# Kernel tuning notes

Hardware: AMD Instinct MI355X
Metric: run time of the kernel (lower is better)

The kernel has to match this reference:

```python
import jax, jax.numpy as jnp
import numpy as np

BETA = 0.95
THRESHOLD = 1.0
ATAN_ALPHA = 2.0  # snntorch default ATan surrogate slope


@jax.custom_vjp
def spike_fn(u):
    # Heaviside spike with ATan surrogate gradient (snntorch default).
    return (u > 0).astype(u.dtype)

def _spike_fwd(u):
    return spike_fn(u), u

def _spike_bwd(u, g):
    grad = (ATAN_ALPHA / 2.0) / (1.0 + (jnp.pi / 2.0 * ATAN_ALPHA * u) ** 2)
    return (g * grad,)

spike_fn.defvjp(_spike_fwd, _spike_bwd)


def setup_inputs() -> dict:
    key = jax.random.key(0)
    k1, k2 = jax.random.split(key)
    x = jax.random.normal(k1, (255, 256, 784), dtype=jnp.float32)
    # Kaiming-ish init for Linear(784, 40, bias=False)
    W = jax.random.normal(k2, (40, 784), dtype=jnp.float32) * (1.0 / np.sqrt(784.0))
    return {"x": x, "W": W}


def reference(x, W):
    # x: [T, B, 784], W: [40, 784]
    B = x.shape[1]
    n_out = W.shape[0]
    mem0 = jnp.zeros((B, n_out), dtype=x.dtype)

    def step(mem, xt):
        cur = xt @ W.T                                  # [B, 40]
        reset = jax.lax.stop_gradient(
            (mem > THRESHOLD).astype(mem.dtype))        # detached, from prev mem
        mem_new = (BETA * mem + cur) * (1.0 - reset)    # zero-reset mechanism
        spk = spike_fn(mem_new - THRESHOLD)
        return mem_new, (spk, mem_new)

    _, (spk_rec, mem_rec) = jax.lax.scan(step, mem0, x)
    return spk_rec, mem_rec  # each [T, B, 40]
```

## Files before the change

### kernel.cpp

```cpp
#include <hip/hip_runtime.h>
#include <hip/hip_bf16.h>

#define T_STEPS 255
#define BATCH 256
#define NIN 784
#define NOUT 40
#define MROWS (T_STEPS * BATCH)
#define TBN (T_STEPS * BATCH * NOUT)
#define BN_CH (BATCH * NOUT)

#define BM 128
#define NCH 25
#define WB_CHUNK 4608
#define EPS_NEAR 2e-4f
#define SCH 30

typedef short bf16x8 __attribute__((ext_vector_type(8)));
typedef float f32x4 __attribute__((ext_vector_type(4)));

__device__ __forceinline__ unsigned short f2bf(float f) {
  unsigned u = __float_as_uint(f);
  u += 0x7fffu + ((u >> 16) & 1u);
  return (unsigned short)(u >> 16);
}
__device__ __forceinline__ float bf2f(unsigned short h) {
  return __uint_as_float(((unsigned)h) << 16);
}

__global__ __launch_bounds__(256) void wsplit_kernel(
    const float* __restrict__ W, unsigned short* __restrict__ Wbg,
    int* __restrict__ count) {
  int i = blockIdx.x * 256 + threadIdx.x;
  if (i == 0) *count = 0;
  if (i >= NCH * WB_CHUNK) return;
  int e = i & 7, l = (i >> 3) & 63, t = (i >> 9) % 3, s = (i / 1536) % 3,
      c = i / 4608;
  int k = c * 32 + (l >> 4) * 8 + e;
  int n = t * 16 + (l & 15);
  float v = (n < NOUT && k < NIN) ? W[n * NIN + k] : 0.f;
  unsigned short h1 = f2bf(v);
  float r1 = v - bf2f(h1);
  unsigned short h2 = f2bf(r1);
  float r2 = r1 - bf2f(h2);
  unsigned short h3 = f2bf(r2);
  Wbg[i] = (s == 0) ? h1 : (s == 1) ? h2 : h3;
}

__global__ __launch_bounds__(256) void lif_gemm_mfma(
    const float* __restrict__ X, const unsigned short* __restrict__ Wbg,
    float* __restrict__ cur) {
  alignas(16) __shared__ float xs0[4096];
  alignas(16) __shared__ float xs1[4096];
  const int tid = threadIdx.x;
  const int m0 = blockIdx.x * BM;
  const int w = tid >> 6, l = tid & 63;
  const int lr = l & 15, lg = l >> 4;

  f32x4 acc[2][3];
#pragma unroll
  for (int st = 0; st < 2; ++st)
#pragma unroll
    for (int t = 0; t < 3; ++t) acc[st][t] = (f32x4){0.f, 0.f, 0.f, 0.f};

  float4 gxA[4], gxB[4];
  bf16x8 BA[9], BB[9];

#define BAR()                                                             \
  do {                                                                    \
    asm volatile("s_waitcnt lgkmcnt(0)" ::: "memory");                    \
    __builtin_amdgcn_s_barrier();                                         \
  } while (0)

#define LOADX(C, DST)                                                     \
  do {                                                                    \
    const int k0_ = (C) * 32;                                             \
    _Pragma("unroll")                                                     \
    for (int i = 0; i < 4; ++i) {                                         \
      int S = tid + i * 256;                                              \
      int row = S >> 3;                                                   \
      int c4 = (S & 7) ^ (row & 7);                                       \
      int k = k0_ + c4 * 4;                                               \
      float4 v = make_float4(0.f, 0.f, 0.f, 0.f);                         \
      if (k < NIN)                                                        \
        v = *reinterpret_cast<const float4*>(X + (size_t)(m0 + row) * NIN + k); \
      DST[i] = v;                                                         \
    }                                                                     \
  } while (0)

#define LOADB(C, DST)                                                     \
  do {                                                                    \
    const unsigned short* base_ = Wbg + (size_t)(C) * WB_CHUNK;           \
    _Pragma("unroll")                                                     \
    for (int q = 0; q < 9; ++q)                                           \
      DST[q] = *reinterpret_cast<const bf16x8*>(base_ + (q * 64 + l) * 8); \
  } while (0)

#define WRITEX(BUF, SRC)                                                  \
  do {                                                                    \
    _Pragma("unroll")                                                     \
    for (int i = 0; i < 4; ++i) {                                         \
      int S = tid + i * 256;                                              \
      *reinterpret_cast<float4*>(&(BUF)[S * 4]) = SRC[i];                 \
    }                                                                     \
  } while (0)

#define COMPUTE(BUF, BSET)                                                \
  do {                                                                    \
    _Pragma("unroll")                                                     \
    for (int st = 0; st < 2; ++st) {                                      \
      int row = (w + st * 4) * 16 + lr;                                   \
      int sA = row * 8 + ((lg * 2) ^ (row & 7));                          \
      int sB = row * 8 + ((lg * 2 + 1) ^ (row & 7));                      \
      float4 fa = *reinterpret_cast<float4*>(&(BUF)[sA * 4]);             \
      float4 fb = *reinterpret_cast<float4*>(&(BUF)[sB * 4]);             \
      float f[8] = {fa.x, fa.y, fa.z, fa.w, fb.x, fb.y, fb.z, fb.w};      \
      union U { unsigned d[4]; bf16x8 v; } A1, A2, A3;                    \
      _Pragma("unroll")                                                   \
      for (int d = 0; d < 4; ++d) {                                       \
        float e0 = f[2 * d], e1 = f[2 * d + 1];                           \
        unsigned u0 = __float_as_uint(e0), u1 = __float_as_uint(e1);      \
        A1.d[d] = __builtin_amdgcn_perm(u1, u0, 0x07060302u);             \
        float r0 = e0 - __uint_as_float(u0 & 0xFFFF0000u);                \
        float r1 = e1 - __uint_as_float(u1 & 0xFFFF0000u);                \
        unsigned v0 = __float_as_uint(r0), v1 = __float_as_uint(r1);      \
        A2.d[d] = __builtin_amdgcn_perm(v1, v0, 0x07060302u);             \
        float s0 = r0 - __uint_as_float(v0 & 0xFFFF0000u);                \
        float s1 = r1 - __uint_as_float(v1 & 0xFFFF0000u);                \
        A3.d[d] = __builtin_amdgcn_perm(__float_as_uint(s1),              \
                                        __float_as_uint(s0), 0x07060302u);\
      }                                                                   \
      _Pragma("unroll")                                                   \
      for (int t = 0; t < 3; ++t) {                                       \
        acc[st][t] = __builtin_amdgcn_mfma_f32_16x16x32_bf16(A3.v, BSET[0 * 3 + t], acc[st][t], 0, 0, 0); \
        acc[st][t] = __builtin_amdgcn_mfma_f32_16x16x32_bf16(A1.v, BSET[2 * 3 + t], acc[st][t], 0, 0, 0); \
        acc[st][t] = __builtin_amdgcn_mfma_f32_16x16x32_bf16(A2.v, BSET[1 * 3 + t], acc[st][t], 0, 0, 0); \
        acc[st][t] = __builtin_amdgcn_mfma_f32_16x16x32_bf16(A2.v, BSET[0 * 3 + t], acc[st][t], 0, 0, 0); \
        acc[st][t] = __builtin_amdgcn_mfma_f32_16x16x32_bf16(A1.v, BSET[1 * 3 + t], acc[st][t], 0, 0, 0); \
        acc[st][t] = __builtin_amdgcn_mfma_f32_16x16x32_bf16(A1.v, BSET[0 * 3 + t], acc[st][t], 0, 0, 0); \
      }                                                                   \
    }                                                                     \
  } while (0)

  LOADX(0, gxA);
  WRITEX(xs0, gxA);
  LOADX(1, gxB);
  LOADB(0, BA);
  LOADB(1, BB);
  BAR();

  for (int c = 0; c < 24; c += 2) {
    if (c + 2 < NCH) LOADX(c + 2, gxA);
    COMPUTE(xs0, BA);
    if (c + 2 < NCH) LOADB(c + 2, BA);
    WRITEX(xs1, gxB);
    BAR();
    if (c + 3 < NCH) LOADX(c + 3, gxB);
    COMPUTE(xs1, BB);
    if (c + 3 < NCH) LOADB(c + 3, BB);
    if (c + 2 < NCH) WRITEX(xs0, gxA);
    BAR();
  }
  COMPUTE(xs0, BA);
#undef LOADX
#undef LOADB
#undef WRITEX
#undef COMPUTE
#undef BAR

#pragma unroll
  for (int st = 0; st < 2; ++st)
#pragma unroll
    for (int t = 0; t < 3; ++t)
#pragma unroll
      for (int r = 0; r < 4; ++r) {
        int col = t * 16 + lr;
        if (col < NOUT) {
          size_t grow = (size_t)m0 + (w + st * 4) * 16 + lg * 4 + r;
          cur[grow * NOUT + col] = acc[st][t][r];
        }
      }
}

__global__ __launch_bounds__(64) void lif_scan_kernel(
    float* __restrict__ spk, float* __restrict__ curmem,
    int* __restrict__ count, int* __restrict__ wlist) {
  const int idx = blockIdx.x * 64 + threadIdx.x;
  float mem = 0.f;
  bool near = false;
  float c[SCH];
#pragma unroll
  for (int i = 0; i < SCH; ++i) c[i] = curmem[(size_t)i * BN_CH + idx];
  for (int ch = 0; ch < 9; ++ch) {
    const int t0 = ch * SCH;
    float nx[SCH];
    if (ch != 8) {
#pragma unroll
      for (int i = 0; i < SCH; ++i) {
        int t = t0 + SCH + i;
        nx[i] = (t < T_STEPS) ? curmem[(size_t)t * BN_CH + idx] : 0.f;
      }
    }
#pragma unroll
    for (int i = 0; i < SCH; ++i) {
      if (t0 + i < T_STEPS) {
        float reset = (mem > 1.0f) ? 1.0f : 0.0f;
        float decay = 0.95f * mem;
        asm volatile("" : "+v"(decay));
        float summ = decay + c[i];
        float mnew = summ * (1.0f - reset);
        near = near || (fabsf(mnew - 1.0f) < EPS_NEAR);
        curmem[(size_t)(t0 + i) * BN_CH + idx] = mnew;
        spk[(size_t)(t0 + i) * BN_CH + idx] = (mnew > 1.0f) ? 1.0f : 0.0f;
        mem = mnew;
      }
    }
    if (ch != 8) {
#pragma unroll
      for (int i = 0; i < SCH; ++i) c[i] = nx[i];
    }
  }
  if (near) {
    int p = atomicAdd(count, 1);
    wlist[p] = idx;
  }
}

__global__ __launch_bounds__(256) void chaindot_kernel(
    const float* __restrict__ X, const float* __restrict__ W,
    const int* __restrict__ count, const int* __restrict__ wlist,
    float* __restrict__ curfix) {
  const int wv0 = blockIdx.x * 4 + (threadIdx.x >> 6);
  const int l = threadIdx.x & 63;
  const int njobs = *count * 32;
  for (int job = wv0; job < njobs; job += 10240) {
    const int f = job >> 5;
    const int tb = (job & 31) * 8;
    const int idx = wlist[f];
    const int b = idx / NOUT, n = idx % NOUT;
    double wreg[13];
#pragma unroll
    for (int j = 0; j < 12; ++j) wreg[j] = (double)W[n * NIN + l + j * 64];
    wreg[12] = (l < 16) ? (double)W[n * NIN + 768 + l] : 0.0;
#pragma unroll
    for (int u = 0; u < 8; ++u) {
      int t = tb + u;
      if (t >= T_STEPS) break;
      const float* xr = X + (size_t)(t * BATCH + b) * NIN;
      double s = 0.0;
#pragma unroll
      for (int j = 0; j < 12; ++j) s = fma((double)xr[l + j * 64], wreg[j], s);
      if (l < 16) s = fma((double)xr[768 + l], wreg[12], s);
#pragma unroll
      for (int off = 32; off; off >>= 1) s += __shfl_xor(s, off);
      if (l == 0) curfix[(size_t)f * T_STEPS + t] = (float)s;
    }
  }
}

__global__ __launch_bounds__(64) void chainscan_kernel(
    float* __restrict__ spk, float* __restrict__ memout,
    const int* __restrict__ count, const int* __restrict__ wlist,
    const float* __restrict__ curfix) {
  const int f = blockIdx.x * 64 + threadIdx.x;
  if (f >= *count) return;
  const int idx = wlist[f];
  const float* cf = curfix + (size_t)f * T_STEPS;
  float mem = 0.f;
  float c[15];
#pragma unroll
  for (int i = 0; i < 15; ++i) c[i] = cf[i];
  for (int ch = 0; ch < 17; ++ch) {
    const int t0 = ch * 15;
    float nx[15];
    if (ch != 16) {
#pragma unroll
      for (int i = 0; i < 15; ++i) nx[i] = cf[t0 + 15 + i];
    }
#pragma unroll
    for (int i = 0; i < 15; ++i) {
      float reset = (mem > 1.0f) ? 1.0f : 0.0f;
      float decay = 0.95f * mem;
      asm volatile("" : "+v"(decay));
      float summ = decay + c[i];
      float mnew = summ * (1.0f - reset);
      spk[(size_t)(t0 + i) * BN_CH + idx] = (mnew > 1.0f) ? 1.0f : 0.0f;
      memout[(size_t)(t0 + i) * BN_CH + idx] = mnew;
      mem = mnew;
    }
    if (ch != 16) {
#pragma unroll
      for (int i = 0; i < 15; ++i) c[i] = nx[i];
    }
  }
}

extern "C" void kernel_launch(void* const* d_in, const int* in_sizes, int n_in,
                              void* d_out, int out_size, void* d_ws,
                              size_t ws_size, hipStream_t stream) {
  (void)in_sizes; (void)n_in; (void)out_size; (void)ws_size;
  const float* X = (const float*)d_in[0];
  const float* W = (const float*)d_in[1];
  float* out = (float*)d_out;
  float* spk = out;
  float* memout = out + TBN;
  char* ws = (char*)d_ws;
  int* count = (int*)ws;
  int* wlist = (int*)(ws + 64);
  unsigned short* Wbg = (unsigned short*)(ws + 41024);
  float* curfix = (float*)(ws + 271424);

  wsplit_kernel<<<(NCH * WB_CHUNK + 255) / 256, 256, 0, stream>>>(W, Wbg,
                                                                  count);
  lif_gemm_mfma<<<MROWS / BM, 256, 0, stream>>>(X, Wbg, memout);
  lif_scan_kernel<<<BN_CH / 64, 64, 0, stream>>>(spk, memout, count, wlist);
  chaindot_kernel<<<2560, 256, 0, stream>>>(X, W, count, wlist, curfix);
  chainscan_kernel<<<BN_CH / 64, 64, 0, stream>>>(spk, memout, count, wlist,
                                                  curfix);
}
```

Measured before the change: 100.1 us.

## Load X fragments directly from global into registers, drop LDS staging and barriers

The GEMM kernel no longer stages X tiles through double-buffered shared memory. Each lane now loads the float4 pairs its MFMA A-fragment needs straight from global memory into registers, using two register sets that alternate chunks. This removes the LDS writes and reads and the workgroup barriers. In exchange, each global load now covers only 32 contiguous bytes per row per lane instead of fully coalesced row segments, which may lower memory efficiency.

```diff
diff --git a/kernel.cpp b/kernel.cpp
--- a/kernel.cpp
+++ b/kernel.cpp
@@ -49,13 +49,14 @@
 __global__ __launch_bounds__(256) void lif_gemm_mfma(
     const float* __restrict__ X, const unsigned short* __restrict__ Wbg,
     float* __restrict__ cur) {
-  alignas(16) __shared__ float xs0[4096];
-  alignas(16) __shared__ float xs1[4096];
   const int tid = threadIdx.x;
   const int m0 = blockIdx.x * BM;
   const int w = tid >> 6, l = tid & 63;
   const int lr = l & 15, lg = l >> 4;
 
+  const float* xp0 = X + (size_t)(m0 + w * 16 + lr) * NIN;
+  const float* xp1 = xp0 + (size_t)64 * NIN;
+
   f32x4 acc[2][3];
 #pragma unroll
   for (int st = 0; st < 2; ++st)
@@ -65,26 +66,21 @@
   float4 gxA[4], gxB[4];
   bf16x8 BA[9], BB[9];
 
-#define BAR()                                                             \
+#define LOADXD(C, DST)                                                    \
   do {                                                                    \
-    asm volatile("s_waitcnt lgkmcnt(0)" ::: "memory");                    \
-    __builtin_amdgcn_s_barrier();                                         \
-  } while (0)
-
-#define LOADX(C, DST)                                                     \
-  do {                                                                    \
-    const int k0_ = (C) * 32;                                             \
-    _Pragma("unroll")                                                     \
-    for (int i = 0; i < 4; ++i) {                                         \
-      int S = tid + i * 256;                                              \
-      int row = S >> 3;                                                   \
-      int c4 = (S & 7) ^ (row & 7);                                       \
-      int k = k0_ + c4 * 4;                                               \
-      float4 v = make_float4(0.f, 0.f, 0.f, 0.f);                         \
-      if (k < NIN)                                                        \
-        v = *reinterpret_cast<const float4*>(X + (size_t)(m0 + row) * NIN + k); \
-      DST[i] = v;                                                         \
-    }                                                                     \
+    const int kb = (C) * 32 + lg * 8;                                     \
+    DST[0] = (kb < NIN)                                                   \
+        ? *reinterpret_cast<const float4*>(xp0 + kb)                      \
+        : make_float4(0.f, 0.f, 0.f, 0.f);                                \
+    DST[1] = (kb + 4 < NIN)                                               \
+        ? *reinterpret_cast<const float4*>(xp0 + kb + 4)                  \
+        : make_float4(0.f, 0.f, 0.f, 0.f);                                \
+    DST[2] = (kb < NIN)                                                   \
+        ? *reinterpret_cast<const float4*>(xp1 + kb)                      \
+        : make_float4(0.f, 0.f, 0.f, 0.f);                                \
+    DST[3] = (kb + 4 < NIN)                                               \
+        ? *reinterpret_cast<const float4*>(xp1 + kb + 4)                  \
+        : make_float4(0.f, 0.f, 0.f, 0.f);                                \
   } while (0)
 
 #define LOADB(C, DST)                                                     \
@@ -95,24 +91,12 @@
       DST[q] = *reinterpret_cast<const bf16x8*>(base_ + (q * 64 + l) * 8); \
   } while (0)
 
-#define WRITEX(BUF, SRC)                                                  \
-  do {                                                                    \
-    _Pragma("unroll")                                                     \
-    for (int i = 0; i < 4; ++i) {                                         \
-      int S = tid + i * 256;                                              \
-      *reinterpret_cast<float4*>(&(BUF)[S * 4]) = SRC[i];                 \
-    }                                                                     \
-  } while (0)
-
-#define COMPUTE(BUF, BSET)                                                \
+#define COMPUTE(GX, BSET)                                                 \
   do {                                                                    \
     _Pragma("unroll")                                                     \
     for (int st = 0; st < 2; ++st) {                                      \
-      int row = (w + st * 4) * 16 + lr;                                   \
-      int sA = row * 8 + ((lg * 2) ^ (row & 7));                          \
-      int sB = row * 8 + ((lg * 2 + 1) ^ (row & 7));                      \
-      float4 fa = *reinterpret_cast<float4*>(&(BUF)[sA * 4]);             \
-      float4 fb = *reinterpret_cast<float4*>(&(BUF)[sB * 4]);             \
+      float4 fa = GX[st * 2];                                             \
+      float4 fb = GX[st * 2 + 1];                                         \
       float f[8] = {fa.x, fa.y, fa.z, fa.w, fb.x, fb.y, fb.z, fb.w};      \
       union U { unsigned d[4]; bf16x8 v; } A1, A2, A3;                    \
       _Pragma("unroll")                                                   \
@@ -141,31 +125,21 @@
     }                                                                     \
   } while (0)
 
-  LOADX(0, gxA);
-  WRITEX(xs0, gxA);
-  LOADX(1, gxB);
+  LOADXD(0, gxA);
   LOADB(0, BA);
+  LOADXD(1, gxB);
   LOADB(1, BB);
-  BAR();
 
   for (int c = 0; c < 24; c += 2) {
-    if (c + 2 < NCH) LOADX(c + 2, gxA);
-    COMPUTE(xs0, BA);
-    if (c + 2 < NCH) LOADB(c + 2, BA);
-    WRITEX(xs1, gxB);
-    BAR();
-    if (c + 3 < NCH) LOADX(c + 3, gxB);
-    COMPUTE(xs1, BB);
-    if (c + 3 < NCH) LOADB(c + 3, BB);
-    if (c + 2 < NCH) WRITEX(xs0, gxA);
-    BAR();
-  }
-  COMPUTE(xs0, BA);
-#undef LOADX
+    COMPUTE(gxA, BA);
+    if (c + 2 < NCH) { LOADXD(c + 2, gxA); LOADB(c + 2, BA); }
+    COMPUTE(gxB, BB);
+    if (c + 3 < NCH) { LOADXD(c + 3, gxB); LOADB(c + 3, BB); }
+  }
+  COMPUTE(gxA, BA);
+#undef LOADXD
 #undef LOADB
-#undef WRITEX
 #undef COMPUTE
-#undef BAR
 
 #pragma unroll
   for (int st = 0; st < 2; ++st)
```

Result: no change. 99.80 us (-0.3%).
